# Kernel tuning notes

Measured on AMD Instinct MI355X. Metric: run time of the kernel, lower is better.

The kernel has to match this reference:

```python
import jax, jax.numpy as jnp
import numpy as np

K_DIM = 1024
N_HEADS = 16
HEAD = K_DIM // N_HEADS


def setup_inputs() -> dict:
    key = jax.random.key(0)
    kx, kq, kk, kv, ko = jax.random.split(key, 5)
    b, t = 2, 2048
    scale = 1.0 / np.sqrt(K_DIM)
    x = jax.random.normal(kx, (b, t, K_DIM), dtype=jnp.float32)
    # nn.Linear(k, k, bias=False): y = x @ W.T, W has shape [k, k]
    Wq = jax.random.normal(kq, (K_DIM, K_DIM), dtype=jnp.float32) * scale
    Wk = jax.random.normal(kk, (K_DIM, K_DIM), dtype=jnp.float32) * scale
    Wv = jax.random.normal(kv, (K_DIM, K_DIM), dtype=jnp.float32) * scale
    Wo = jax.random.normal(ko, (K_DIM, K_DIM), dtype=jnp.float32) * scale
    return {"x": x, "Wq": Wq, "Wk": Wk, "Wv": Wv, "Wo": Wo}


def reference(x, Wq, Wk, Wv, Wo):
    b, t, k = x.shape
    h, hs = N_HEADS, HEAD
    # projections (torch Linear: x @ W.T), split heads -> [b, h, t, hs]
    Q = (x @ Wq.T).reshape(b, t, h, hs).transpose(0, 2, 1, 3)
    Kt = (x @ Wk.T).reshape(b, t, h, hs).transpose(0, 2, 1, 3)
    V = (x @ Wv.T).reshape(b, t, h, hs).transpose(0, 2, 1, 3)
    # NOTE: original scales by sqrt(k) (model dim), not sqrt(head_size)
    scores = jnp.einsum('bhqd,bhkd->bhqk', Q, Kt) / jnp.sqrt(jnp.asarray(k, x.dtype))
    W = jax.nn.softmax(scores, axis=-1)
    O = jnp.einsum('bhqk,bhkd->bhqd', W, V)  # [b, h, t, hs]
    O = O.transpose(0, 2, 1, 3).reshape(b, t, k)
    return O @ Wo.T
```

## Files before the change

kernel.cpp:

```cpp
#include <hip/hip_runtime.h>
#include <hip/hip_bf16.h>

#define N_HEADS 16
#define HEAD 64
#define B_SZ 2
#define T_SZ 2048
#define KD 1024
#define M_TOT (B_SZ * T_SZ)

typedef short bf16x8 __attribute__((ext_vector_type(8)));
typedef short bf16x4 __attribute__((ext_vector_type(4)));
typedef float f32x4  __attribute__((ext_vector_type(4)));

#define MFMA32(a, b, c) __builtin_amdgcn_mfma_f32_16x16x32_bf16((a), (b), (c), 0, 0, 0)

__device__ __forceinline__ bf16x8 cat8(bf16x4 lo, bf16x4 hi) {
    return __builtin_shufflevector(lo, hi, 0, 1, 2, 3, 4, 5, 6, 7);
}

__device__ __forceinline__ ushort f2bf(float f) {
    __hip_bfloat16 h = __float2bfloat16(f);
    return *reinterpret_cast<ushort*>(&h);
}

__device__ __forceinline__ ushort f2bf_fast(float f) {
    return (ushort)((__float_as_uint(f) + 0x8000u) >> 16);
}

__device__ __forceinline__ float exp2fast(float x) {
#if __has_builtin(__builtin_amdgcn_exp2f)
    return __builtin_amdgcn_exp2f(x);
#else
    return exp2f(x);
#endif
}

__device__ __forceinline__ void gl2lds16(const ushort* g, void* l) {
    __builtin_amdgcn_global_load_lds(
        (const __attribute__((address_space(1))) unsigned int*)g,
        (__attribute__((address_space(3))) unsigned int*)l, 16, 0, 0);
}

#define RAW_BARRIER() do { asm volatile("" ::: "memory"); \
                           __builtin_amdgcn_s_barrier();  \
                           asm volatile("" ::: "memory"); } while (0)

__global__ void cvt_all(const float* __restrict__ x,
                        const float* __restrict__ Wq, const float* __restrict__ Wk,
                        const float* __restrict__ Wv, const float* __restrict__ Wo,
                        ushort* __restrict__ xb, ushort* __restrict__ wb) {
    const int NX = (M_TOT * KD) / 4;
    const int NW = (KD * KD) / 4;
    int i = blockIdx.x * blockDim.x + threadIdx.x;
    float4 v;
    ushort* dst;
    if (i < NX) {
        v = reinterpret_cast<const float4*>(x)[i];
        dst = xb + (size_t)i * 4;
    } else {
        int j = i - NX;
        int w = j >> 18;
        int r = j & (NW - 1);
        const float* s = (w == 0) ? Wq : (w == 1) ? Wk : (w == 2) ? Wv : Wo;
        v = reinterpret_cast<const float4*>(s)[r];
        dst = wb + (size_t)w * KD * KD + (size_t)r * 4;
    }
    ushort4 o;
    o.x = f2bf(v.x); o.y = f2bf(v.y); o.z = f2bf(v.z); o.w = f2bf(v.w);
    *reinterpret_cast<ushort4*>(dst) = o;
}

__global__ __launch_bounds__(256) void gemm_qkv(const ushort* __restrict__ A,
                                                const ushort* __restrict__ Bm,
                                                ushort* __restrict__ Qbase) {
    const int bm = blockIdx.x;
    const int bn = blockIdx.y;
    __shared__ alignas(128) char As[2][16384];
    __shared__ alignas(128) char Bs[2][16384];
    const int tid = threadIdx.x;
    const int lane = tid & 63;
    const int w = tid >> 6;
    const int wr = w >> 1, wc = w & 1;
    const int r15 = lane & 15, q4 = lane >> 4;
    const int sl8 = lane >> 3;
    const int scol = (((lane & 7) * 16) ^ (sl8 << 4)) >> 1;

    f32x4 acc[4][4] = {};

    #define GSTAGE(buf, k0)                                                          \
        {                                                                            \
            _Pragma("unroll")                                                        \
            for (int rr = 0; rr < 4; ++rr) {                                         \
                int r = rr * 32 + w * 8 + sl8;                                       \
                gl2lds16(A  + (size_t)(bm * 128 + r) * 1024 + (k0) + scol,           \
                         &As[buf][(rr * 32 + w * 8) * 128]);                         \
                gl2lds16(Bm + (size_t)(bn * 128 + r) * 1024 + (k0) + scol,           \
                         &Bs[buf][(rr * 32 + w * 8) * 128]);                         \
            }                                                                        \
        }

    GSTAGE(0, 0);
    int cur = 0;
    for (int t = 0; t < 16; ++t) {
        GSTAGE(cur ^ 1, ((t + 1) & 15) * 64);
        asm volatile("s_waitcnt vmcnt(8)" ::: "memory");
        RAW_BARRIER();

        #pragma unroll
        for (int kk = 0; kk < 2; ++kk) {
            bf16x8 af[4], bfr[4];
            #pragma unroll
            for (int m = 0; m < 4; ++m) {
                int row = wr * 64 + m * 16 + r15;
                af[m] = *(const bf16x8*)(&As[cur][row * 128 + ((kk * 64 + q4 * 16) ^ ((row & 7) << 4))]);
            }
            #pragma unroll
            for (int n = 0; n < 4; ++n) {
                int row = wc * 64 + n * 16 + r15;
                bfr[n] = *(const bf16x8*)(&Bs[cur][row * 128 + ((kk * 64 + q4 * 16) ^ ((row & 7) << 4))]);
            }
            #pragma unroll
            for (int m = 0; m < 4; ++m)
                #pragma unroll
                for (int n = 0; n < 4; ++n)
                    acc[m][n] = MFMA32(af[m], bfr[n], acc[m][n]);
        }
        RAW_BARRIER();
        cur ^= 1;
    }
    #undef GSTAGE
    asm volatile("s_waitcnt vmcnt(0)" ::: "memory");
    RAW_BARRIER();

    const size_t seg = (size_t)32 * 2048 * 64;
    const int which = bn >> 3;
    const int row0 = bm * 128 + wr * 64;
    const int col0w = bn * 128 + wc * 64;

    if (which == 2) {
        #pragma unroll
        for (int m = 0; m < 4; ++m)
            #pragma unroll
            for (int n = 0; n < 4; ++n) {
                int col = col0w + n * 16 + r15;
                int rem = col & 1023;
                int head = rem >> 6;
                int d = rem & 63;
                int row_base = row0 + m * 16 + q4 * 4;
                int bidx = row_base >> 11;
                int t = row_base & 2047;
                int bh_ = bidx * 16 + head;
                ushort4 o;
                o.x = f2bf(acc[m][n][0]); o.y = f2bf(acc[m][n][1]);
                o.z = f2bf(acc[m][n][2]); o.w = f2bf(acc[m][n][3]);
                *(ushort4*)(&Qbase[2 * seg + ((size_t)bh_ * 64 + d) * 2048 + t]) = o;
            }
    } else {
        const float sc = (which == 0) ? 0.045084439f : 1.0f;
        char* ep = (char*)As + w * 8192;
        #pragma unroll
        for (int m = 0; m < 4; ++m)
            #pragma unroll
            for (int n = 0; n < 4; ++n)
                #pragma unroll
                for (int i = 0; i < 4; ++i) {
                    int row = m * 16 + q4 * 4 + i;
                    int dby = (n * 16 + r15) * 2;
                    *(ushort*)(ep + row * 128 + (dby ^ ((row & 7) << 4))) =
                        f2bf(acc[m][n][i] * sc);
                }
        const int head = (col0w & 1023) >> 6;
        #pragma unroll
        for (int j = 0; j < 8; ++j) {
            int row = (lane >> 3) + j * 8;
            bf16x8 vv = *(const bf16x8*)(ep + row * 128 +
                                         (((lane & 7) * 16) ^ ((row & 7) << 4)));
            int grow = row0 + row;
            int bidx = grow >> 11;
            int t = grow & 2047;
            *(bf16x8*)(&Qbase[(size_t)which * seg +
                              (((size_t)(bidx * 16 + head) * 2048 + t) * 64) + (lane & 7) * 8]) = vv;
        }
    }
}

__global__ __launch_bounds__(256) void gemm_o(const ushort* __restrict__ A,
                                              const ushort* __restrict__ Bm,
                                              float* __restrict__ C) {
    const int bm = blockIdx.x;
    const int bn = blockIdx.y;
    __shared__ alignas(128) char As[2][16384];
    __shared__ alignas(128) char Bs[2][8192];
    const int tid = threadIdx.x;
    const int lane = tid & 63;
    const int w = tid >> 6;
    const int wr = w >> 1, wc = w & 1;
    const int r15 = lane & 15, q4 = lane >> 4;
    const int sl8 = lane >> 3;
    const int scol = (((lane & 7) * 16) ^ (sl8 << 4)) >> 1;

    f32x4 acc[4][2] = {};

    #define OSTAGE(buf, k0)                                                          \
        {                                                                            \
            _Pragma("unroll")                                                        \
            for (int rr = 0; rr < 4; ++rr) {                                         \
                int r = w * 32 + rr * 8 + sl8;                                       \
                gl2lds16(A + (size_t)(bm * 128 + r) * 1024 + (k0) + scol,            \
                         &As[buf][(w * 32 + rr * 8) * 128]);                         \
            }                                                                        \
            _Pragma("unroll")                                                        \
            for (int rr = 0; rr < 2; ++rr) {                                         \
                int r = w * 16 + rr * 8 + sl8;                                       \
                gl2lds16(Bm + (size_t)(bn * 64 + r) * 1024 + (k0) + scol,            \
                         &Bs[buf][(w * 16 + rr * 8) * 128]);                         \
            }                                                                        \
        }

    OSTAGE(0, 0);
    int cur = 0;
    for (int t = 0; t < 16; ++t) {
        OSTAGE(cur ^ 1, ((t + 1) & 15) * 64);
        asm volatile("s_waitcnt vmcnt(6)" ::: "memory");
        RAW_BARRIER();

        #pragma unroll
        for (int kk = 0; kk < 2; ++kk) {
            bf16x8 af[4], bfr[2];
            #pragma unroll
            for (int m = 0; m < 4; ++m) {
                int row = wr * 64 + m * 16 + r15;
                af[m] = *(const bf16x8*)(&As[cur][row * 128 + ((kk * 64 + q4 * 16) ^ ((row & 7) << 4))]);
            }
            #pragma unroll
            for (int n = 0; n < 2; ++n) {
                int row = wc * 32 + n * 16 + r15;
                bfr[n] = *(const bf16x8*)(&Bs[cur][row * 128 + ((kk * 64 + q4 * 16) ^ ((row & 7) << 4))]);
            }
            #pragma unroll
            for (int m = 0; m < 4; ++m)
                #pragma unroll
                for (int n = 0; n < 2; ++n)
                    acc[m][n] = MFMA32(af[m], bfr[n], acc[m][n]);
        }
        RAW_BARRIER();
        cur ^= 1;
    }
    #undef OSTAGE
    asm volatile("s_waitcnt vmcnt(0)" ::: "memory");

    const int row0 = bm * 128 + wr * 64;
    const int col0 = bn * 64 + wc * 32;
    #pragma unroll
    for (int m = 0; m < 4; ++m)
        #pragma unroll
        for (int n = 0; n < 2; ++n)
            #pragma unroll
            for (int i = 0; i < 4; ++i)
                C[(size_t)(row0 + m * 16 + q4 * 4 + i) * 1024 + col0 + n * 16 + r15] =
                    acc[m][n][i];
}

__global__ __launch_bounds__(1024) void attn_fwd(const ushort* __restrict__ Qh,
                                                 const ushort* __restrict__ Kh,
                                                 const ushort* __restrict__ Vt,
                                                 ushort* __restrict__ Ob) {
    const int bh = blockIdx.x;
    const int qt = blockIdx.y;
    const int tid = threadIdx.x;
    const int lane = tid & 63, w = tid >> 6;
    const int grp = w >> 3, wl = w & 7;
    const int r15 = lane & 15, q4 = lane >> 4;

    const ushort* Qp = Qh + (size_t)bh * T_SZ * HEAD;
    const ushort* Kp = Kh + (size_t)bh * T_SZ * HEAD;
    const ushort* Vp = Vt + (size_t)bh * HEAD * T_SZ;

    __shared__ alignas(16) char SMEM[65536];
    char* Kbuf = SMEM + grp * 32768;
    char* Vbuf = Kbuf + 16384;

    const int srow = wl * 8 + (lane >> 3);
    const int sslot = (lane & 7) * 16;
    const int ssb = (sslot ^ ((srow & 7) << 4)) >> 1;
    const int kvbase = grp << 10;

    const int q0 = qt * 256 + wl * 32;
    bf16x8 qf[2][2];
    #pragma unroll
    for (int cc = 0; cc < 2; ++cc) {
        qf[cc][0] = *(const bf16x8*)(&Qp[(size_t)(q0 + cc * 16 + r15) * 64 + q4 * 8]);
        qf[cc][1] = *(const bf16x8*)(&Qp[(size_t)(q0 + cc * 16 + r15) * 64 + 32 + q4 * 8]);
    }

    float l_[2] = {0.f, 0.f};
    f32x4 acc[2][4] = {};

    #define STAGE(buf, kv0)                                                      \
        {                                                                        \
            gl2lds16(Kp + (size_t)(kvbase + (kv0) + srow) * 64 + ssb,            \
                     Kbuf + (buf) * 8192 + wl * 8 * 128);                        \
            gl2lds16(Vp + (size_t)srow * 2048 + kvbase + (kv0) + ssb,            \
                     Vbuf + (buf) * 8192 + wl * 8 * 128);                        \
        }

    STAGE(0, 0);
    int cur = 0;
    for (int it = 0; it < 16; ++it) {
        STAGE(cur ^ 1, ((it + 1) & 15) * 64);
        asm volatile("s_waitcnt vmcnt(2)" ::: "memory");
        RAW_BARRIER();

        const char* Ks = Kbuf + cur * 8192;
        const char* Vs = Vbuf + cur * 8192;

        bf16x8 kf[4][2];
        #pragma unroll
        for (int t4 = 0; t4 < 4; ++t4) {
            int row = t4 * 16 + r15;
            int sw = (row & 7) << 4;
            kf[t4][0] = *(const bf16x8*)(&Ks[row * 128 + ((q4 * 16) ^ sw)]);
            kf[t4][1] = *(const bf16x8*)(&Ks[row * 128 + ((64 + q4 * 16) ^ sw)]);
        }
        bf16x4 vf[4][4];
        #pragma unroll
        for (int dt = 0; dt < 4; ++dt) {
            int row = dt * 16 + r15;
            int sw = (row & 7) << 4;
            #pragma unroll
            for (int t4 = 0; t4 < 4; ++t4)
                vf[t4][dt] = *(const bf16x4*)(&Vs[row * 128 + ((t4 * 32 + q4 * 8) ^ sw)]);
        }

        f32x4 z[2][4];
        #pragma unroll
        for (int cc = 0; cc < 2; ++cc)
            #pragma unroll
            for (int t4 = 0; t4 < 4; ++t4) {
                f32x4 zz = {};
                zz = MFMA32(kf[t4][0], qf[cc][0], zz);
                zz = MFMA32(kf[t4][1], qf[cc][1], zz);
                z[cc][t4] = zz;
            }

        bf16x4 pb[2][4];
        #pragma unroll
        for (int cc = 0; cc < 2; ++cc) {
            float rst[4];
            #pragma unroll
            for (int t4 = 0; t4 < 4; ++t4) {
                float p0 = exp2fast(z[cc][t4][0]);
                float p1 = exp2fast(z[cc][t4][1]);
                float p2 = exp2fast(z[cc][t4][2]);
                float p3 = exp2fast(z[cc][t4][3]);
                pb[cc][t4][0] = (short)f2bf_fast(p0);
                pb[cc][t4][1] = (short)f2bf_fast(p1);
                pb[cc][t4][2] = (short)f2bf_fast(p2);
                pb[cc][t4][3] = (short)f2bf_fast(p3);
                rst[t4] = (p0 + p1) + (p2 + p3);
            }
            l_[cc] += (rst[0] + rst[1]) + (rst[2] + rst[3]);
        }

        #pragma unroll
        for (int t32 = 0; t32 < 2; ++t32)
            #pragma unroll
            for (int dt = 0; dt < 4; ++dt) {
                bf16x8 a8 = cat8(vf[2 * t32][dt], vf[2 * t32 + 1][dt]);
                #pragma unroll
                for (int cc = 0; cc < 2; ++cc)
                    acc[cc][dt] = MFMA32(a8, cat8(pb[cc][2 * t32], pb[cc][2 * t32 + 1]),
                                         acc[cc][dt]);
            }

        RAW_BARRIER();
        cur ^= 1;
    }
    #undef STAGE

    asm volatile("s_waitcnt vmcnt(0)" ::: "memory");
    __syncthreads();

    {
        float* MB = (float*)SMEM;
        #pragma unroll
        for (int rnd = 0; rnd < 2; ++rnd) {
            __syncthreads();
            if (grp == 1 && (wl >> 2) == rnd) {
                float* p = MB + (((wl & 3) * 64 + lane) * 34);
                #pragma unroll
                for (int cc = 0; cc < 2; ++cc)
                    #pragma unroll
                    for (int dt = 0; dt < 4; ++dt) {
                        *(float2*)(p + (cc * 4 + dt) * 4)     = make_float2(acc[cc][dt][0], acc[cc][dt][1]);
                        *(float2*)(p + (cc * 4 + dt) * 4 + 2) = make_float2(acc[cc][dt][2], acc[cc][dt][3]);
                    }
                *(float2*)(p + 32) = make_float2(l_[0], l_[1]);
            }
            __syncthreads();
            if (grp == 0 && (wl >> 2) == rnd) {
                const float* p = MB + (((wl & 3) * 64 + lane) * 34);
                #pragma unroll
                for (int cc = 0; cc < 2; ++cc)
                    #pragma unroll
                    for (int dt = 0; dt < 4; ++dt)
                        #pragma unroll
                        for (int i = 0; i < 4; ++i)
                            acc[cc][dt][i] += p[(cc * 4 + dt) * 4 + i];
                l_[0] += p[32];
                l_[1] += p[33];
            }
        }
    }

    if (grp == 0) {
        const int b = bh >> 4, h = bh & 15;
        #pragma unroll
        for (int cc = 0; cc < 2; ++cc) {
            float lf = l_[cc];
            lf += __shfl_xor(lf, 16, 64);
            lf += __shfl_xor(lf, 32, 64);
            float inv = 1.0f / lf;
            int q = q0 + cc * 16 + r15;
            #pragma unroll
            for (int dt = 0; dt < 4; ++dt) {
                ushort4 o;
                o.x = f2bf(acc[cc][dt][0] * inv);
                o.y = f2bf(acc[cc][dt][1] * inv);
                o.z = f2bf(acc[cc][dt][2] * inv);
                o.w = f2bf(acc[cc][dt][3] * inv);
                *(ushort4*)(&Ob[((size_t)(b * T_SZ + q)) * KD + h * HEAD + dt * 16 + q4 * 4]) = o;
            }
        }
    }
}

extern "C" void kernel_launch(void* const* d_in, const int* in_sizes, int n_in,
                              void* d_out, int out_size, void* d_ws, size_t ws_size,
                              hipStream_t stream) {
    const float* x  = (const float*)d_in[0];
    const float* Wq = (const float*)d_in[1];
    const float* Wk = (const float*)d_in[2];
    const float* Wv = (const float*)d_in[3];
    const float* Wo = (const float*)d_in[4];

    char* ws = (char*)d_ws;
    const size_t MB = 1024 * 1024;
    ushort* xb    = (ushort*)(ws + 0);
    ushort* Wqkvb = (ushort*)(ws + 8  * MB);
    ushort* Wob   = Wqkvb + 3 * (size_t)KD * KD;
    ushort* Qh    = (ushort*)(ws + 16 * MB);
    ushort* Kh    = (ushort*)(ws + 24 * MB);
    ushort* VhT   = (ushort*)(ws + 32 * MB);
    ushort* Ob    = (ushort*)(ws + 40 * MB);

    {
        int total4 = (M_TOT * KD) / 4 + KD * KD;
        cvt_all<<<total4 / 256, 256, 0, stream>>>(x, Wq, Wk, Wv, Wo, xb, Wqkvb);
    }

    gemm_qkv<<<dim3(32, 24), 256, 0, stream>>>(xb, Wqkvb, Qh);
    attn_fwd<<<dim3(32, 8), 1024, 0, stream>>>(Qh, Kh, VhT, Ob);
    gemm_o<<<dim3(32, 16), 256, 0, stream>>>(Ob, Wob, (float*)d_out);
}
```

Measured before the change: 109.5 us.

## Permute V layout for 16-byte fragment loads and compute softmax row sums via MFMA

The projection epilogue now writes the transposed V with a permutation of 4-element blocks inside each 32-token chunk. This lets the attention kernel load each V operand as one 16-byte bf16x8 read instead of two 8-byte reads plus a shuffle. The softmax denominator is now accumulated by an extra MFMA against a vector of ones instead of scalar adds and cross-lane shuffles, which trades VALU work for extra matrix instructions. Correctness depends on the permutation matching between producer and consumer.

```diff
diff --git a/kernel.cpp b/kernel.cpp
--- a/kernel.cpp
+++ b/kernel.cpp
@@ -13,10 +13,6 @@
 typedef float f32x4  __attribute__((ext_vector_type(4)));
 
 #define MFMA32(a, b, c) __builtin_amdgcn_mfma_f32_16x16x32_bf16((a), (b), (c), 0, 0, 0)
-
-__device__ __forceinline__ bf16x8 cat8(bf16x4 lo, bf16x4 hi) {
-    return __builtin_shufflevector(lo, hi, 0, 1, 2, 3, 4, 5, 6, 7);
-}
 
 __device__ __forceinline__ ushort f2bf(float f) {
     __hip_bfloat16 h = __float2bfloat16(f);
@@ -150,10 +146,13 @@
                 int bidx = row_base >> 11;
                 int t = row_base & 2047;
                 int bh_ = bidx * 16 + head;
+                int blk = (t >> 2) & 7;
+                int npos = (blk < 4) ? (blk << 1) : ((blk << 1) - 7);
+                int tp = (t & ~31) | (npos << 2);
                 ushort4 o;
                 o.x = f2bf(acc[m][n][0]); o.y = f2bf(acc[m][n][1]);
                 o.z = f2bf(acc[m][n][2]); o.w = f2bf(acc[m][n][3]);
-                *(ushort4*)(&Qbase[2 * seg + ((size_t)bh_ * 64 + d) * 2048 + t]) = o;
+                *(ushort4*)(&Qbase[2 * seg + ((size_t)bh_ * 64 + d) * 2048 + tp]) = o;
             }
     } else {
         const float sc = (which == 0) ? 0.045084439f : 1.0f;
@@ -293,8 +292,10 @@
         qf[cc][1] = *(const bf16x8*)(&Qp[(size_t)(q0 + cc * 16 + r15) * 64 + 32 + q4 * 8]);
     }
 
-    float l_[2] = {0.f, 0.f};
+    const bf16x8 ones8 = {0x3F80, 0x3F80, 0x3F80, 0x3F80, 0x3F80, 0x3F80, 0x3F80, 0x3F80};
+
     f32x4 acc[2][4] = {};
+    f32x4 acc_l[2] = {};
 
     #define STAGE(buf, kv0)                                                      \
         {                                                                        \
@@ -322,14 +323,14 @@
             kf[t4][0] = *(const bf16x8*)(&Ks[row * 128 + ((q4 * 16) ^ sw)]);
             kf[t4][1] = *(const bf16x8*)(&Ks[row * 128 + ((64 + q4 * 16) ^ sw)]);
         }
-        bf16x4 vf[4][4];
+        bf16x8 vf8[2][4];
         #pragma unroll
         for (int dt = 0; dt < 4; ++dt) {
             int row = dt * 16 + r15;
             int sw = (row & 7) << 4;
             #pragma unroll
-            for (int t4 = 0; t4 < 4; ++t4)
-                vf[t4][dt] = *(const bf16x4*)(&Vs[row * 128 + ((t4 * 32 + q4 * 8) ^ sw)]);
+            for (int t32 = 0; t32 < 2; ++t32)
+                vf8[t32][dt] = *(const bf16x8*)(&Vs[row * 128 + ((t32 * 64 + q4 * 16) ^ sw)]);
         }
 
         f32x4 z[2][4];
@@ -343,35 +344,28 @@
                 z[cc][t4] = zz;
             }
 
-        bf16x4 pb[2][4];
-        #pragma unroll
-        for (int cc = 0; cc < 2; ++cc) {
-            float rst[4];
-            #pragma unroll
-            for (int t4 = 0; t4 < 4; ++t4) {
-                float p0 = exp2fast(z[cc][t4][0]);
-                float p1 = exp2fast(z[cc][t4][1]);
-                float p2 = exp2fast(z[cc][t4][2]);
-                float p3 = exp2fast(z[cc][t4][3]);
-                pb[cc][t4][0] = (short)f2bf_fast(p0);
-                pb[cc][t4][1] = (short)f2bf_fast(p1);
-                pb[cc][t4][2] = (short)f2bf_fast(p2);
-                pb[cc][t4][3] = (short)f2bf_fast(p3);
-                rst[t4] = (p0 + p1) + (p2 + p3);
-            }
-            l_[cc] += (rst[0] + rst[1]) + (rst[2] + rst[3]);
-        }
-
-        #pragma unroll
-        for (int t32 = 0; t32 < 2; ++t32)
-            #pragma unroll
-            for (int dt = 0; dt < 4; ++dt) {
-                bf16x8 a8 = cat8(vf[2 * t32][dt], vf[2 * t32 + 1][dt]);
+        bf16x8 pb8[2][2];
+        #pragma unroll
+        for (int cc = 0; cc < 2; ++cc)
+            #pragma unroll
+            for (int t32 = 0; t32 < 2; ++t32)
+                #pragma unroll
+                for (int i = 0; i < 4; ++i) {
+                    pb8[cc][t32][i]     = (short)f2bf_fast(exp2fast(z[cc][2 * t32][i]));
+                    pb8[cc][t32][4 + i] = (short)f2bf_fast(exp2fast(z[cc][2 * t32 + 1][i]));
+                }
+
+        #pragma unroll
+        for (int t32 = 0; t32 < 2; ++t32) {
+            #pragma unroll
+            for (int dt = 0; dt < 4; ++dt)
                 #pragma unroll
                 for (int cc = 0; cc < 2; ++cc)
-                    acc[cc][dt] = MFMA32(a8, cat8(pb[cc][2 * t32], pb[cc][2 * t32 + 1]),
-                                         acc[cc][dt]);
-            }
+                    acc[cc][dt] = MFMA32(vf8[t32][dt], pb8[cc][t32], acc[cc][dt]);
+            #pragma unroll
+            for (int cc = 0; cc < 2; ++cc)
+                acc_l[cc] = MFMA32(ones8, pb8[cc][t32], acc_l[cc]);
+        }
 
         RAW_BARRIER();
         cur ^= 1;
@@ -381,6 +375,7 @@
     asm volatile("s_waitcnt vmcnt(0)" ::: "memory");
     __syncthreads();
 
+    float l0 = acc_l[0][0], l1 = acc_l[1][0];
     {
         float* MB = (float*)SMEM;
         #pragma unroll
@@ -395,7 +390,7 @@
                         *(float2*)(p + (cc * 4 + dt) * 4)     = make_float2(acc[cc][dt][0], acc[cc][dt][1]);
                         *(float2*)(p + (cc * 4 + dt) * 4 + 2) = make_float2(acc[cc][dt][2], acc[cc][dt][3]);
                     }
-                *(float2*)(p + 32) = make_float2(l_[0], l_[1]);
+                *(float2*)(p + 32) = make_float2(l0, l1);
             }
             __syncthreads();
             if (grp == 0 && (wl >> 2) == rnd) {
@@ -407,8 +402,8 @@
                         #pragma unroll
                         for (int i = 0; i < 4; ++i)
                             acc[cc][dt][i] += p[(cc * 4 + dt) * 4 + i];
-                l_[0] += p[32];
-                l_[1] += p[33];
+                l0 += p[32];
+                l1 += p[33];
             }
         }
     }
@@ -417,10 +412,7 @@
         const int b = bh >> 4, h = bh & 15;
         #pragma unroll
         for (int cc = 0; cc < 2; ++cc) {
-            float lf = l_[cc];
-            lf += __shfl_xor(lf, 16, 64);
-            lf += __shfl_xor(lf, 32, 64);
-            float inv = 1.0f / lf;
+            float inv = 1.0f / (cc ? l1 : l0);
             int q = q0 + cc * 16 + r15;
             #pragma unroll
             for (int dt = 0; dt < 4; ++dt) {
```

After: 105.0 us. 1.04x faster.
